# Kernel tuning notes

Hardware: AMD Instinct MI355X
Metric: run time of the kernel (lower is better)

## Reference

```python
import jax, jax.numpy as jnp
import numpy as np

B, IN_CH, N, DIM, PH, HID, K = 4, 128, 2048, 256, 64, 1024, 16
EPS = 1e-5


def conv1(x, w, b):
    # 1x1 Conv1d: x (B,C,N), w (O,C) -> (B,O,N)
    return jnp.einsum('oc,bcn->bon', w, x) + b[None, :, None]


def conv2(x, w, b):
    # 1x1 Conv2d: x (B,C,N,K), w (O,C) -> (B,O,N,K)
    return jnp.einsum('oc,bcnk->bonk', w, x) + b[None, :, None, None]


def bn2(x, g, beta, mean, var):
    # eval-mode BatchNorm2d over channel dim of (B,C,N,K)
    scale = g * jax.lax.rsqrt(var + EPS)
    return x * scale[None, :, None, None] + (beta - mean * scale)[None, :, None, None]


def query_knn(pos, k):
    # pos: (B,3,N). Returns (B,N,K) indices of k nearest neighbors (incl. self).
    p = jnp.transpose(pos, (0, 2, 1))                     # (B,N,3)
    sq = jnp.sum(p * p, axis=-1)                          # (B,N)
    dist = sq[:, :, None] + sq[:, None, :] - 2.0 * jnp.einsum('bnc,bmc->bnm', p, p)
    _, idx = jax.lax.top_k(-dist, k)                      # smallest distances first
    return idx


def group(feat, idx):
    # feat: (B,C,N), idx: (B,N,K) -> (B,C,N,K) where out[b,c,i,k]=feat[b,c,idx[b,i,k]]
    b, c, n = feat.shape
    k = idx.shape[-1]
    ib = jnp.broadcast_to(idx.reshape(b, 1, n * k), (b, c, n * k))
    return jnp.take_along_axis(feat, ib, axis=2).reshape(b, c, n, k)


def setup_inputs() -> dict:
    key = jax.random.key(0)
    ks = jax.random.split(key, 12)
    s = 0.02
    return {
        'x': jax.random.normal(ks[0], (B, IN_CH, N), jnp.float32),
        'pos': jax.random.normal(ks[1], (B, 3, N), jnp.float32),
        'ls_w': jax.random.normal(ks[2], (DIM, IN_CH), jnp.float32) * s,
        'ls_b': jnp.zeros((DIM,), jnp.float32),
        'kw': jax.random.normal(ks[3], (DIM, DIM), jnp.float32) * s,
        'kb': jnp.zeros((DIM,), jnp.float32),
        'qw': jax.random.normal(ks[4], (DIM, DIM), jnp.float32) * s,
        'qb': jnp.zeros((DIM,), jnp.float32),
        'vw': jax.random.normal(ks[5], (DIM, DIM), jnp.float32) * s,
        'vb': jnp.zeros((DIM,), jnp.float32),
        'pw1': jax.random.normal(ks[6], (PH, 3), jnp.float32) * s,
        'pb1': jnp.zeros((PH,), jnp.float32),
        'pg': jnp.ones((PH,), jnp.float32),
        'pbeta': jnp.zeros((PH,), jnp.float32),
        'pmean': jnp.zeros((PH,), jnp.float32),
        'pvar': jnp.ones((PH,), jnp.float32),
        'pw2': jax.random.normal(ks[7], (DIM, PH), jnp.float32) * s,
        'pb2': jnp.zeros((DIM,), jnp.float32),
        'aw1': jax.random.normal(ks[8], (HID, DIM), jnp.float32) * s,
        'ab1': jnp.zeros((HID,), jnp.float32),
        'ag': jnp.ones((HID,), jnp.float32),
        'abeta': jnp.zeros((HID,), jnp.float32),
        'amean': jnp.zeros((HID,), jnp.float32),
        'avar': jnp.ones((HID,), jnp.float32),
        'aw2': jax.random.normal(ks[9], (DIM, HID), jnp.float32) * s,
        'ab2': jnp.zeros((DIM,), jnp.float32),
        'lw': jax.random.normal(ks[10], (IN_CH, DIM), jnp.float32) * s,
        'lb': jnp.zeros((IN_CH,), jnp.float32),
    }


def reference(x, pos, ls_w, ls_b, kw, kb, qw, qb, vw, vb,
              pw1, pb1, pg, pbeta, pmean, pvar, pw2, pb2,
              aw1, ab1, ag, abeta, amean, avar, aw2, ab2, lw, lb):
    identity = x
    h = conv1(x, ls_w, ls_b)                              # (B,DIM,N)
    idx = query_knn(pos, K)                               # (B,N,K) int32
    key_f = group(conv1(h, kw, kb), idx)                  # (B,DIM,N,K)
    value = conv1(h, vw, vb)                              # (B,DIM,N)
    query = conv1(h, qw, qb)                              # (B,DIM,N)
    qk_rel = query[:, :, :, None] - key_f                 # (B,DIM,N,K)
    pos_rel = pos[:, :, :, None] - group(pos, idx)        # (B,3,N,K)
    pe = conv2(jax.nn.relu(bn2(conv2(pos_rel, pw1, pb1), pg, pbeta, pmean, pvar)), pw2, pb2)
    attn = conv2(jax.nn.relu(bn2(conv2(qk_rel + pe, aw1, ab1), ag, abeta, amean, avar)), aw2, ab2)
    attn = jax.nn.softmax(attn, axis=-1)                  # softmax over K
    val_g = group(value, idx) + pe                        # (B,DIM,N,K)
    agg = jnp.sum(attn * val_g, axis=-1)                  # (B,DIM,N)
    y = conv1(agg, lw, lb)                                # (B,IN_CH,N)
    return y + identity
```

## Files before the change

kernel.cpp:

```cpp
#include <hip/hip_runtime.h>
#include <hip/hip_bf16.h>
#include <math.h>

#define B_    4
#define CIN   128
#define NPTS  2048
#define DIM   256
#define PH    64
#define HIDN  1024
#define KNN_  16
#define BN    (B_*NPTS)
#define CC    (BN*KNN_)
#define QKV   768
#define EPS_  1e-5f

typedef __bf16 bf16;
typedef __bf16 bf16x8 __attribute__((ext_vector_type(8)));
typedef __bf16 bf16x4 __attribute__((ext_vector_type(4)));
typedef float  f32x4  __attribute__((ext_vector_type(4)));

__global__ __launch_bounds__(256) void prep_kernel(
    const float* __restrict__ ls_w, const float* __restrict__ qw,
    const float* __restrict__ kw,   const float* __restrict__ vw,
    const float* __restrict__ pw2,  const float* __restrict__ aw1,
    const float* __restrict__ aw2,  const float* __restrict__ lw,
    const float* __restrict__ qb,   const float* __restrict__ kb,
    const float* __restrict__ vb,
    const float* __restrict__ pb1,  const float* __restrict__ pg,
    const float* __restrict__ pbeta,const float* __restrict__ pmean,
    const float* __restrict__ pvar,
    const float* __restrict__ ab1,  const float* __restrict__ ag,
    const float* __restrict__ abeta,const float* __restrict__ amean,
    const float* __restrict__ avar,
    bf16* ls_wb, bf16* wqkvb, bf16* pw2b, bf16* aw1b, bf16* aw2b, bf16* lwb,
    float* pe_scale, float* pe_shift, float* at_scale, float* at_shift,
    float* bqkv)
{
  long e = (long)blockIdx.x * 256 + threadIdx.x;
  if (e < 32768)  { ls_wb[e] = (bf16)ls_w[e]; return; } e -= 32768;
  if (e < 196608) {
    int row = (int)(e >> 8), col = (int)(e & 255);
    float v = (row < 256) ? qw[row * 256 + col]
            : (row < 512) ? kw[(row - 256) * 256 + col]
                          : vw[(row - 512) * 256 + col];
    wqkvb[e] = (bf16)v; return;
  } e -= 196608;
  if (e < 16384)  { pw2b[e] = (bf16)pw2[e];  return; } e -= 16384;
  if (e < 262144) { aw1b[e] = (bf16)aw1[e];  return; } e -= 262144;
  if (e < 262144) { aw2b[e] = (bf16)aw2[e];  return; } e -= 262144;
  if (e < 32768)  { lwb[e]  = (bf16)lw[e];   return; } e -= 32768;
  if (e < 64) {
    float sc = pg[e] * rsqrtf(pvar[e] + EPS_);
    pe_scale[e] = sc;
    pe_shift[e] = sc * pb1[e] + pbeta[e] - pmean[e] * sc;
    return;
  } e -= 64;
  if (e < 1024) {
    float sc = ag[e] * rsqrtf(avar[e] + EPS_);
    at_scale[e] = sc;
    at_shift[e] = sc * ab1[e] + abeta[e] - amean[e] * sc;
    return;
  } e -= 1024;
  if (e < 768) {
    bqkv[e] = (e < 256) ? qb[e] : (e < 512) ? kb[e - 256] : vb[e - 512];
  }
}

__global__ __launch_bounds__(256) void transpose_x_kernel(
    const float* __restrict__ x, bf16* __restrict__ xT)
{
  long e = (long)blockIdx.x * 256 + threadIdx.x;
  int ch = (int)(e & (CIN - 1));
  long i = e >> 7;
  int n = (int)(i & (NPTS - 1));
  int b = (int)(i >> 11);
  xT[e] = (bf16)x[((long)b * CIN + ch) * NPTS + n];
}

__global__ __launch_bounds__(256) void knn_kernel(
    const float* __restrict__ pos, int* __restrict__ idx_out)
{
  __shared__ float px[NPTS], py[NPTS], pz[NPTS];
  const int tid = threadIdx.x;
  const int lane = tid & 63, wave = tid >> 6;
  const int q = blockIdx.x * 4 + wave;
  const int b = q >> 11;
  const int n = q & (NPTS - 1);
  const float* p = pos + (long)b * 3 * NPTS;
  for (int j = tid; j < NPTS; j += 256) {
    px[j] = p[j]; py[j] = p[NPTS + j]; pz[j] = p[2 * NPTS + j];
  }
  __syncthreads();
  float qx = px[n], qy = py[n], qz = pz[n];
  float qs = qx * qx + qy * qy + qz * qz;
  float d[32];
#pragma unroll
  for (int j = 0; j < 32; ++j) {
    int pt = j * 64 + lane;
    float x = px[pt], y = py[pt], z = pz[pt];
    float s2 = x * x + y * y + z * z;
    float dt = qx * x + qy * y + qz * z;
    d[j] = qs + s2 - 2.f * dt;
  }
  for (int r = 0; r < KNN_; ++r) {
    float bv = 1e30f; int bj = 0;
#pragma unroll
    for (int j = 0; j < 32; ++j)
      if (d[j] < bv) { bv = d[j]; bj = j; }
    int bi = bj * 64 + lane;
#pragma unroll
    for (int off = 32; off >= 1; off >>= 1) {
      float ov = __shfl_xor(bv, off);
      int   oi = __shfl_xor(bi, off);
      if (ov < bv || (ov == bv && oi < bi)) { bv = ov; bi = oi; }
    }
    if (lane == 0) idx_out[(long)q * KNN_ + r] = bi;
#pragma unroll
    for (int j = 0; j < 32; ++j)
      if (bi == j * 64 + lane) d[j] = 1e30f;
  }
}

template<int KD, bool OBF16>
__global__ __launch_bounds__(256) void gemmT_kernel(
    const bf16* __restrict__ inT, const bf16* __restrict__ Wb,
    const float* __restrict__ bias, void* __restrict__ outp, int O)
{
  const int tid = threadIdx.x;
  const int lane = tid & 63, wave = tid >> 6;
  const int row16 = lane & 15, grp = lane >> 4;
  const long i0 = (long)blockIdx.x * 64 + (wave & 1) * 32;
  const long o0 = (long)blockIdx.y * 64 + (wave >> 1) * 32;
  f32x4 acc[2][2] = {};
  const bf16* a0p = inT + (i0 + row16) * KD + grp * 8;
  const bf16* a1p = a0p + 16 * KD;
  const bf16* b0p = Wb + (o0 + row16) * KD + grp * 8;
  const bf16* b1p = b0p + 16 * KD;
#pragma unroll
  for (int ks = 0; ks < KD / 32; ++ks) {
    bf16x8 a0 = *(const bf16x8*)(a0p + ks * 32);
    bf16x8 a1 = *(const bf16x8*)(a1p + ks * 32);
    bf16x8 b0 = *(const bf16x8*)(b0p + ks * 32);
    bf16x8 b1 = *(const bf16x8*)(b1p + ks * 32);
    acc[0][0] = __builtin_amdgcn_mfma_f32_16x16x32_bf16(a0, b0, acc[0][0], 0, 0, 0);
    acc[0][1] = __builtin_amdgcn_mfma_f32_16x16x32_bf16(a0, b1, acc[0][1], 0, 0, 0);
    acc[1][0] = __builtin_amdgcn_mfma_f32_16x16x32_bf16(a1, b0, acc[1][0], 0, 0, 0);
    acc[1][1] = __builtin_amdgcn_mfma_f32_16x16x32_bf16(a1, b1, acc[1][1], 0, 0, 0);
  }
#pragma unroll
  for (int ot = 0; ot < 2; ++ot) {
    long o = o0 + ot * 16 + row16;
    float bv = bias[o];
#pragma unroll
    for (int it = 0; it < 2; ++it) {
#pragma unroll
      for (int r = 0; r < 4; ++r) {
        long i = i0 + it * 16 + grp * 4 + r;
        float v = acc[it][ot][r] + bv;
        if (OBF16) ((bf16*)outp)[i * O + o] = (bf16)v;
        else       ((float*)outp)[i * O + o] = v;
      }
    }
  }
}

__global__ __launch_bounds__(256) void gemmT_qkv_kernel(
    const bf16* __restrict__ inT, const bf16* __restrict__ Wb,
    const float* __restrict__ bias,
    bf16* __restrict__ qTb, bf16* __restrict__ kTb, bf16* __restrict__ vTb)
{
  const int tid = threadIdx.x;
  const int lane = tid & 63, wave = tid >> 6;
  const int row16 = lane & 15, grp = lane >> 4;
  const long i0 = (long)blockIdx.x * 64 + (wave & 1) * 32;
  const long o0 = (long)blockIdx.y * 64 + (wave >> 1) * 32;
  f32x4 acc[2][2] = {};
  const bf16* a0p = inT + (i0 + row16) * DIM + grp * 8;
  const bf16* a1p = a0p + 16 * DIM;
  const bf16* b0p = Wb + (o0 + row16) * DIM + grp * 8;
  const bf16* b1p = b0p + 16 * DIM;
#pragma unroll
  for (int ks = 0; ks < 8; ++ks) {
    bf16x8 a0 = *(const bf16x8*)(a0p + ks * 32);
    bf16x8 a1 = *(const bf16x8*)(a1p + ks * 32);
    bf16x8 b0 = *(const bf16x8*)(b0p + ks * 32);
    bf16x8 b1 = *(const bf16x8*)(b1p + ks * 32);
    acc[0][0] = __builtin_amdgcn_mfma_f32_16x16x32_bf16(a0, b0, acc[0][0], 0, 0, 0);
    acc[0][1] = __builtin_amdgcn_mfma_f32_16x16x32_bf16(a0, b1, acc[0][1], 0, 0, 0);
    acc[1][0] = __builtin_amdgcn_mfma_f32_16x16x32_bf16(a1, b0, acc[1][0], 0, 0, 0);
    acc[1][1] = __builtin_amdgcn_mfma_f32_16x16x32_bf16(a1, b1, acc[1][1], 0, 0, 0);
  }
#pragma unroll
  for (int ot = 0; ot < 2; ++ot) {
    long o = o0 + ot * 16 + row16;
    int third = (int)(o >> 8);
    bf16* outp = third == 0 ? qTb : third == 1 ? kTb : vTb;
    int oo = (int)(o & 255);
    float bv = bias[o];
#pragma unroll
    for (int it = 0; it < 2; ++it) {
#pragma unroll
      for (int r = 0; r < 4; ++r) {
        long i = i0 + it * 16 + grp * 4 + r;
        outp[i * DIM + oo] = (bf16)(acc[it][ot][r] + bv);
      }
    }
  }
}

__global__ __launch_bounds__(256, 3) void attn_fused_kernel(
    const bf16* __restrict__ qTb, const bf16* __restrict__ kTb,
    const bf16* __restrict__ vTb, const float* __restrict__ pos,
    const int* __restrict__ idx, const float* __restrict__ pw1,
    const float* __restrict__ pe_scale, const float* __restrict__ pe_shift,
    const bf16* __restrict__ pw2b, const float* __restrict__ pb2,
    const bf16* __restrict__ aw1b, const bf16* __restrict__ aw2b,
    const float* __restrict__ at_scale, const float* __restrict__ at_shift,
    const float* __restrict__ ab2, bf16* __restrict__ aggT)
{
  __shared__ __align__(16) bf16 u_lds[64][272];
  __shared__ __align__(16) bf16 tbuf[64 * 136];
  __shared__ float rel_lds[64][4];
  __shared__ int   idx_lds[64];
  bf16 (*t_lds)[136]  = (bf16(*)[136])tbuf;
  bf16 (*hid_lds)[72] = (bf16(*)[72])tbuf;

  const int tid = threadIdx.x;
  const int lane = tid & 63, wave = tid >> 6;
  const int row16 = lane & 15, grp = lane >> 4;
  const long c0 = (long)blockIdx.x * 64;
  const int bn0 = blockIdx.x * 4;
  const int b = bn0 >> 11;
  const float* pB = pos + (long)b * 3 * NPTS;
  const int os = wave * 64;
  const int hs = wave * 32;

  if (tid < 64) {
    int nb = idx[c0 + tid];
    idx_lds[tid] = nb;
    int n = (bn0 + (tid >> 4)) & (NPTS - 1);
    rel_lds[tid][0] = pB[n] - pB[nb];
    rel_lds[tid][1] = pB[NPTS + n] - pB[NPTS + nb];
    rel_lds[tid][2] = pB[2 * NPTS + n] - pB[2 * NPTS + nb];
  }
  __syncthreads();

  {
    int c = tid & 63, jq = tid >> 6;
    float rx = rel_lds[c][0], ry = rel_lds[c][1], rz = rel_lds[c][2];
#pragma unroll
    for (int jj = 0; jj < 16; ++jj) {
      int j = jq * 16 + jj;
      float v = pw1[j * 3] * rx + pw1[j * 3 + 1] * ry + pw1[j * 3 + 2] * rz;
      v = pe_scale[j] * v + pe_shift[j];
      hid_lds[c][j] = (bf16)fmaxf(v, 0.f);
    }
  }
  __syncthreads();

  {
    bf16x8 bw[2][4];
#pragma unroll
    for (int ks = 0; ks < 2; ++ks)
#pragma unroll
      for (int ot = 0; ot < 4; ++ot)
        bw[ks][ot] = *(const bf16x8*)(pw2b + (long)(os + ot * 16 + row16) * PH + ks * 32 + grp * 8);
#pragma unroll
    for (int ct = 0; ct < 4; ++ct) {
      f32x4 aT[4] = {};
#pragma unroll
      for (int ks = 0; ks < 2; ++ks) {
        bf16x8 ah = *(const bf16x8*)&hid_lds[ct * 16 + row16][ks * 32 + grp * 8];
#pragma unroll
        for (int ot = 0; ot < 4; ++ot)
          aT[ot] = __builtin_amdgcn_mfma_f32_16x16x32_bf16(bw[ks][ot], ah, aT[ot], 0, 0, 0);
      }
      int nb = idx_lds[ct * 16 + row16];
      const bf16* krow = kTb + ((long)b * NPTS + nb) * DIM + os;
      const bf16* qrow = qTb + (long)(bn0 + ct) * DIM + os;
#pragma unroll
      for (int ot = 0; ot < 4; ++ot) {
        int o4 = ot * 16 + grp * 4;
        bf16x4 k4 = *(const bf16x4*)(krow + o4);
        bf16x4 q4 = *(const bf16x4*)(qrow + o4);
        f32x4 pb4 = *(const f32x4*)&pb2[os + o4];
        bf16x4 u4;
#pragma unroll
        for (int r = 0; r < 4; ++r)
          u4[r] = (bf16)((float)q4[r] - (float)k4[r] + aT[ot][r] + pb4[r]);
        *(bf16x4*)&u_lds[ct * 16 + row16][os + o4] = u4;
      }
    }
  }
  __syncthreads();

  f32x4 acc2[4][4] = {};
  for (int jc = 0; jc < 8; ++jc) {
    const int hg = jc * 128 + hs;
#pragma unroll
    for (int jt = 0; jt < 2; ++jt) {
      f32x4 acc1[4] = {};
#pragma unroll
      for (int ks = 0; ks < 8; ++ks) {
        bf16x8 aw = *(const bf16x8*)(aw1b + (long)(hg + jt * 16 + row16) * DIM + ks * 32 + grp * 8);
#pragma unroll
        for (int ct = 0; ct < 4; ++ct) {
          bf16x8 bu = *(const bf16x8*)&u_lds[ct * 16 + row16][ks * 32 + grp * 8];
          acc1[ct] = __builtin_amdgcn_mfma_f32_16x16x32_bf16(aw, bu, acc1[ct], 0, 0, 0);
        }
      }
      int jb = hg + jt * 16 + grp * 4;
      f32x4 sc4 = *(const f32x4*)&at_scale[jb];
      f32x4 sh4 = *(const f32x4*)&at_shift[jb];
#pragma unroll
      for (int ct = 0; ct < 4; ++ct) {
        bf16x4 pk;
#pragma unroll
        for (int r = 0; r < 4; ++r) {
          float v = sc4[r] * acc1[ct][r] + sh4[r];
          pk[r] = (bf16)fmaxf(v, 0.f);
        }
        *(bf16x4*)&t_lds[ct * 16 + row16][hs + jt * 16 + grp * 4] = pk;
      }
    }
    __syncthreads();
#pragma unroll
    for (int ks2 = 0; ks2 < 4; ++ks2) {
      bf16x8 a2[4], b2;
#pragma unroll
      for (int ct = 0; ct < 4; ++ct)
        a2[ct] = *(const bf16x8*)&t_lds[ct * 16 + row16][ks2 * 32 + grp * 8];
#pragma unroll
      for (int ot = 0; ot < 4; ++ot) {
        b2 = *(const bf16x8*)(aw2b + (long)(os + ot * 16 + row16) * HIDN + jc * 128 + ks2 * 32 + grp * 8);
#pragma unroll
        for (int ct = 0; ct < 4; ++ct)
          acc2[ct][ot] = __builtin_amdgcn_mfma_f32_16x16x32_bf16(a2[ct], b2, acc2[ct][ot], 0, 0, 0);
      }
    }
    __syncthreads();
  }

  {
    int c = tid & 63, jq = tid >> 6;
    float rx = rel_lds[c][0], ry = rel_lds[c][1], rz = rel_lds[c][2];
#pragma unroll
    for (int jj = 0; jj < 16; ++jj) {
      int j = jq * 16 + jj;
      float v = pw1[j * 3] * rx + pw1[j * 3 + 1] * ry + pw1[j * 3 + 2] * rz;
      v = pe_scale[j] * v + pe_shift[j];
      hid_lds[c][j] = (bf16)fmaxf(v, 0.f);
    }
  }
  __syncthreads();

#pragma unroll
  for (int ct = 0; ct < 4; ++ct) {
    f32x4 accpe[4] = {};
#pragma unroll
    for (int ks = 0; ks < 2; ++ks) {
      bf16x8 ah = *(const bf16x8*)&hid_lds[ct * 16 + row16][ks * 32 + grp * 8];
#pragma unroll
      for (int ot = 0; ot < 4; ++ot) {
        bf16x8 bwv = *(const bf16x8*)(pw2b + (long)(os + ot * 16 + row16) * PH + ks * 32 + grp * 8);
        accpe[ot] = __builtin_amdgcn_mfma_f32_16x16x32_bf16(ah, bwv, accpe[ot], 0, 0, 0);
      }
    }
#pragma unroll
    for (int ot = 0; ot < 4; ++ot) {
      int o = os + ot * 16 + row16;
      float ab = ab2[o];
      float pb2v = pb2[o];
      float l[4];
      float m = -1e30f;
#pragma unroll
      for (int r = 0; r < 4; ++r) {
        l[r] = acc2[ct][ot][r] + ab;
        m = fmaxf(m, l[r]);
      }
      m = fmaxf(m, __shfl_xor(m, 16));
      m = fmaxf(m, __shfl_xor(m, 32));
      float s = 0.f;
#pragma unroll
      for (int r = 0; r < 4; ++r) { l[r] = expf(l[r] - m); s += l[r]; }
      s += __shfl_xor(s, 16);
      s += __shfl_xor(s, 32);
      float inv = 1.f / s;
      float agg = 0.f;
#pragma unroll
      for (int r = 0; r < 4; ++r) {
        int c = ct * 16 + grp * 4 + r;
        int nb = idx_lds[c];
        float vv = (float)vTb[((long)b * NPTS + nb) * DIM + o];
        agg += l[r] * (vv + accpe[ot][r] + pb2v);
      }
      agg *= inv;
      agg += __shfl_xor(agg, 16);
      agg += __shfl_xor(agg, 32);
      if (grp == 0) aggT[(long)(bn0 + ct) * DIM + o] = (bf16)agg;
    }
  }
}

__global__ __launch_bounds__(256) void final_kernel(
    const bf16* __restrict__ aggT, const bf16* __restrict__ lwb,
    const float* __restrict__ lb, const float* __restrict__ x,
    float* __restrict__ out)
{
  const int tid = threadIdx.x;
  const int lane = tid & 63, wave = tid >> 6;
  const int row16 = lane & 15, grp = lane >> 4;
  const long i0 = (long)blockIdx.x * 64 + (wave & 1) * 32;
  const int o0 = blockIdx.y * 64 + (wave >> 1) * 32;
  f32x4 acc[2][2] = {};
  const bf16* a0p = aggT + (i0 + row16) * DIM + grp * 8;
  const bf16* a1p = a0p + 16 * DIM;
  const bf16* b0p = lwb + (long)(o0 + row16) * DIM + grp * 8;
  const bf16* b1p = b0p + 16 * DIM;
#pragma unroll
  for (int ks = 0; ks < 8; ++ks) {
    bf16x8 a0 = *(const bf16x8*)(a0p + ks * 32);
    bf16x8 a1 = *(const bf16x8*)(a1p + ks * 32);
    bf16x8 b0 = *(const bf16x8*)(b0p + ks * 32);
    bf16x8 b1 = *(const bf16x8*)(b1p + ks * 32);
    acc[0][0] = __builtin_amdgcn_mfma_f32_16x16x32_bf16(a0, b0, acc[0][0], 0, 0, 0);
    acc[0][1] = __builtin_amdgcn_mfma_f32_16x16x32_bf16(a0, b1, acc[0][1], 0, 0, 0);
    acc[1][0] = __builtin_amdgcn_mfma_f32_16x16x32_bf16(a1, b0, acc[1][0], 0, 0, 0);
    acc[1][1] = __builtin_amdgcn_mfma_f32_16x16x32_bf16(a1, b1, acc[1][1], 0, 0, 0);
  }
#pragma unroll
  for (int ot = 0; ot < 2; ++ot) {
    int o = o0 + ot * 16 + row16;
    float bv = lb[o];
#pragma unroll
    for (int it = 0; it < 2; ++it) {
#pragma unroll
      for (int r = 0; r < 4; ++r) {
        long i = i0 + it * 16 + grp * 4 + r;
        int bb = (int)(i >> 11);
        int n = (int)(i & (NPTS - 1));
        long off = ((long)bb * CIN + o) * NPTS + n;
        out[off] = acc[it][ot][r] + bv + x[off];
      }
    }
  }
}

extern "C" void kernel_launch(void* const* d_in, const int* in_sizes, int n_in,
                              void* d_out, int out_size, void* d_ws, size_t ws_size,
                              hipStream_t stream)
{
  const float* x     = (const float*)d_in[0];
  const float* pos   = (const float*)d_in[1];
  const float* ls_w  = (const float*)d_in[2];
  const float* ls_b  = (const float*)d_in[3];
  const float* kw    = (const float*)d_in[4];
  const float* kb    = (const float*)d_in[5];
  const float* qw    = (const float*)d_in[6];
  const float* qb    = (const float*)d_in[7];
  const float* vw    = (const float*)d_in[8];
  const float* vb    = (const float*)d_in[9];
  const float* pw1   = (const float*)d_in[10];
  const float* pb1   = (const float*)d_in[11];
  const float* pg    = (const float*)d_in[12];
  const float* pbeta = (const float*)d_in[13];
  const float* pmean = (const float*)d_in[14];
  const float* pvar  = (const float*)d_in[15];
  const float* pw2   = (const float*)d_in[16];
  const float* pb2   = (const float*)d_in[17];
  const float* aw1   = (const float*)d_in[18];
  const float* ab1   = (const float*)d_in[19];
  const float* ag    = (const float*)d_in[20];
  const float* abeta = (const float*)d_in[21];
  const float* amean = (const float*)d_in[22];
  const float* avar  = (const float*)d_in[23];
  const float* aw2   = (const float*)d_in[24];
  const float* ab2   = (const float*)d_in[25];
  const float* lw    = (const float*)d_in[26];
  const float* lb    = (const float*)d_in[27];

  char* ws = (char*)d_ws;
  size_t off = 0;
  auto alloc = [&](size_t bytes) -> void* {
    void* p = ws + off;
    off = (off + bytes + 255) & ~(size_t)255;
    return p;
  };

  bf16* ls_wb = (bf16*)alloc(32768 * 2);
  bf16* wqkvb = (bf16*)alloc(196608 * 2);
  bf16* pw2b  = (bf16*)alloc(16384 * 2);
  bf16* aw1b  = (bf16*)alloc(262144 * 2);
  bf16* aw2b  = (bf16*)alloc(262144 * 2);
  bf16* lwb   = (bf16*)alloc(32768 * 2);
  float* pe_scale = (float*)alloc(64 * 4);
  float* pe_shift = (float*)alloc(64 * 4);
  float* at_scale = (float*)alloc(1024 * 4);
  float* at_shift = (float*)alloc(1024 * 4);
  float* bqkv = (float*)alloc(768 * 4);
  int*  idx  = (int*)alloc((size_t)CC * 4);
  bf16* xT   = (bf16*)alloc((size_t)BN * CIN * 2);
  bf16* hT   = (bf16*)alloc((size_t)BN * DIM * 2);
  bf16* qTb  = (bf16*)alloc((size_t)BN * DIM * 2);
  bf16* kTb  = (bf16*)alloc((size_t)BN * DIM * 2);
  bf16* vTb  = (bf16*)alloc((size_t)BN * DIM * 2);
  bf16* aggT = (bf16*)alloc((size_t)BN * DIM * 2);

  prep_kernel<<<dim3((804672 + 255) / 256), 256, 0, stream>>>(
      ls_w, qw, kw, vw, pw2, aw1, aw2, lw, qb, kb, vb,
      pb1, pg, pbeta, pmean, pvar, ab1, ag, abeta, amean, avar,
      ls_wb, wqkvb, pw2b, aw1b, aw2b, lwb,
      pe_scale, pe_shift, at_scale, at_shift, bqkv);

  transpose_x_kernel<<<dim3(BN * CIN / 256), 256, 0, stream>>>(x, xT);

  knn_kernel<<<dim3(BN / 4), 256, 0, stream>>>(pos, idx);

  gemmT_kernel<128, true><<<dim3(BN / 64, DIM / 64), 256, 0, stream>>>(xT, ls_wb, ls_b, hT, DIM);

  gemmT_qkv_kernel<<<dim3(BN / 64, QKV / 64), 256, 0, stream>>>(hT, wqkvb, bqkv, qTb, kTb, vTb);

  attn_fused_kernel<<<dim3(CC / 64), 256, 0, stream>>>(
      qTb, kTb, vTb, pos, idx, pw1, pe_scale, pe_shift, pw2b, pb2,
      aw1b, aw2b, at_scale, at_shift, ab2, aggT);

  final_kernel<<<dim3(BN / 64, CIN / 64), 256, 0, stream>>>(aggT, lwb, lb, x, (float*)d_out);
}
```

Baseline: 555.9 us.

## Switch attention MLP GEMMs to FP8 MFMA with fp8 weights and activations

Converts aw1/aw2 weights to fp8 e4m3 in prep and quantises the u and hidden activations to fp8 in LDS, using fp8 16x16x32 MFMA instead of bf16. Hidden chunks widen from 128 to 256 columns, halving barrier count. This cuts memory and LDS bytes and uses the higher-rate fp8 matrix path, but adds quantisation error that may exceed tolerance.

```diff
diff --git a/kernel.cpp b/kernel.cpp
--- a/kernel.cpp
+++ b/kernel.cpp
@@ -18,6 +18,14 @@
 typedef __bf16 bf16x8 __attribute__((ext_vector_type(8)));
 typedef __bf16 bf16x4 __attribute__((ext_vector_type(4)));
 typedef float  f32x4  __attribute__((ext_vector_type(4)));
+typedef unsigned char u8;
+typedef long long i64;
+
+static __device__ __forceinline__ int pack4_fp8(float a, float b, float c, float d) {
+  int v = __builtin_amdgcn_cvt_pk_fp8_f32(a, b, 0, false);
+  v = __builtin_amdgcn_cvt_pk_fp8_f32(c, d, v, true);
+  return v;
+}
 
 __global__ __launch_bounds__(256) void prep_kernel(
     const float* __restrict__ ls_w, const float* __restrict__ qw,
@@ -32,7 +40,7 @@
     const float* __restrict__ ab1,  const float* __restrict__ ag,
     const float* __restrict__ abeta,const float* __restrict__ amean,
     const float* __restrict__ avar,
-    bf16* ls_wb, bf16* wqkvb, bf16* pw2b, bf16* aw1b, bf16* aw2b, bf16* lwb,
+    bf16* ls_wb, bf16* wqkvb, bf16* pw2b, u8* aw1f8, u8* aw2f8, bf16* lwb,
     float* pe_scale, float* pe_shift, float* at_scale, float* at_shift,
     float* bqkv)
 {
@@ -46,8 +54,14 @@
     wqkvb[e] = (bf16)v; return;
   } e -= 196608;
   if (e < 16384)  { pw2b[e] = (bf16)pw2[e];  return; } e -= 16384;
-  if (e < 262144) { aw1b[e] = (bf16)aw1[e];  return; } e -= 262144;
-  if (e < 262144) { aw2b[e] = (bf16)aw2[e];  return; } e -= 262144;
+  if (e < 262144) {
+    int p = __builtin_amdgcn_cvt_pk_fp8_f32(aw1[e], 0.f, 0, false);
+    aw1f8[e] = (u8)p; return;
+  } e -= 262144;
+  if (e < 262144) {
+    int p = __builtin_amdgcn_cvt_pk_fp8_f32(aw2[e], 0.f, 0, false);
+    aw2f8[e] = (u8)p; return;
+  } e -= 262144;
   if (e < 32768)  { lwb[e]  = (bf16)lw[e];   return; } e -= 32768;
   if (e < 64) {
     float sc = pg[e] * rsqrtf(pvar[e] + EPS_);
@@ -214,15 +228,15 @@
     const int* __restrict__ idx, const float* __restrict__ pw1,
     const float* __restrict__ pe_scale, const float* __restrict__ pe_shift,
     const bf16* __restrict__ pw2b, const float* __restrict__ pb2,
-    const bf16* __restrict__ aw1b, const bf16* __restrict__ aw2b,
+    const u8* __restrict__ aw1f8, const u8* __restrict__ aw2f8,
     const float* __restrict__ at_scale, const float* __restrict__ at_shift,
     const float* __restrict__ ab2, bf16* __restrict__ aggT)
 {
-  __shared__ __align__(16) bf16 u_lds[64][272];
-  __shared__ __align__(16) bf16 tbuf[64 * 136];
+  __shared__ __align__(16) u8 u_lds[64][264];
+  __shared__ __align__(16) u8 tbuf[64 * 264];
   __shared__ float rel_lds[64][4];
   __shared__ int   idx_lds[64];
-  bf16 (*t_lds)[136]  = (bf16(*)[136])tbuf;
+  u8   (*t_lds)[264]  = (u8(*)[264])tbuf;
   bf16 (*hid_lds)[72] = (bf16(*)[72])tbuf;
 
   const int tid = threadIdx.x;
@@ -233,7 +247,7 @@
   const int b = bn0 >> 11;
   const float* pB = pos + (long)b * 3 * NPTS;
   const int os = wave * 64;
-  const int hs = wave * 32;
+  const int hs = wave * 64;
 
   if (tid < 64) {
     int nb = idx[c0 + tid];
@@ -284,58 +298,58 @@
         bf16x4 k4 = *(const bf16x4*)(krow + o4);
         bf16x4 q4 = *(const bf16x4*)(qrow + o4);
         f32x4 pb4 = *(const f32x4*)&pb2[os + o4];
-        bf16x4 u4;
-#pragma unroll
-        for (int r = 0; r < 4; ++r)
-          u4[r] = (bf16)((float)q4[r] - (float)k4[r] + aT[ot][r] + pb4[r]);
-        *(bf16x4*)&u_lds[ct * 16 + row16][os + o4] = u4;
+        int u32 = pack4_fp8(
+            (float)q4[0] - (float)k4[0] + aT[ot][0] + pb4[0],
+            (float)q4[1] - (float)k4[1] + aT[ot][1] + pb4[1],
+            (float)q4[2] - (float)k4[2] + aT[ot][2] + pb4[2],
+            (float)q4[3] - (float)k4[3] + aT[ot][3] + pb4[3]);
+        *(int*)&u_lds[ct * 16 + row16][os + o4] = u32;
       }
     }
   }
   __syncthreads();
 
   f32x4 acc2[4][4] = {};
-  for (int jc = 0; jc < 8; ++jc) {
-    const int hg = jc * 128 + hs;
-#pragma unroll
-    for (int jt = 0; jt < 2; ++jt) {
+  for (int jc = 0; jc < 4; ++jc) {
+#pragma unroll
+    for (int jt = 0; jt < 4; ++jt) {
+      const int jrow = jc * 256 + hs + jt * 16 + row16;
       f32x4 acc1[4] = {};
 #pragma unroll
       for (int ks = 0; ks < 8; ++ks) {
-        bf16x8 aw = *(const bf16x8*)(aw1b + (long)(hg + jt * 16 + row16) * DIM + ks * 32 + grp * 8);
+        i64 aw = *(const i64*)(aw1f8 + (long)jrow * DIM + ks * 32 + grp * 8);
 #pragma unroll
         for (int ct = 0; ct < 4; ++ct) {
-          bf16x8 bu = *(const bf16x8*)&u_lds[ct * 16 + row16][ks * 32 + grp * 8];
-          acc1[ct] = __builtin_amdgcn_mfma_f32_16x16x32_bf16(aw, bu, acc1[ct], 0, 0, 0);
+          i64 bu = *(const i64*)&u_lds[ct * 16 + row16][ks * 32 + grp * 8];
+          acc1[ct] = __builtin_amdgcn_mfma_f32_16x16x32_fp8_fp8(aw, bu, acc1[ct], 0, 0, 0);
         }
       }
-      int jb = hg + jt * 16 + grp * 4;
+      int jb = jc * 256 + hs + jt * 16 + grp * 4;
       f32x4 sc4 = *(const f32x4*)&at_scale[jb];
       f32x4 sh4 = *(const f32x4*)&at_shift[jb];
 #pragma unroll
       for (int ct = 0; ct < 4; ++ct) {
-        bf16x4 pk;
-#pragma unroll
-        for (int r = 0; r < 4; ++r) {
-          float v = sc4[r] * acc1[ct][r] + sh4[r];
-          pk[r] = (bf16)fmaxf(v, 0.f);
-        }
-        *(bf16x4*)&t_lds[ct * 16 + row16][hs + jt * 16 + grp * 4] = pk;
+        int pk = pack4_fp8(
+            fmaxf(sc4[0] * acc1[ct][0] + sh4[0], 0.f),
+            fmaxf(sc4[1] * acc1[ct][1] + sh4[1], 0.f),
+            fmaxf(sc4[2] * acc1[ct][2] + sh4[2], 0.f),
+            fmaxf(sc4[3] * acc1[ct][3] + sh4[3], 0.f));
+        *(int*)&t_lds[ct * 16 + row16][hs + jt * 16 + grp * 4] = pk;
       }
     }
     __syncthreads();
 #pragma unroll
-    for (int ks2 = 0; ks2 < 4; ++ks2) {
-      bf16x8 a2[4], b2;
+    for (int ks2 = 0; ks2 < 8; ++ks2) {
+      i64 a2[4];
 #pragma unroll
       for (int ct = 0; ct < 4; ++ct)
-        a2[ct] = *(const bf16x8*)&t_lds[ct * 16 + row16][ks2 * 32 + grp * 8];
+        a2[ct] = *(const i64*)&t_lds[ct * 16 + row16][ks2 * 32 + grp * 8];
 #pragma unroll
       for (int ot = 0; ot < 4; ++ot) {
-        b2 = *(const bf16x8*)(aw2b + (long)(os + ot * 16 + row16) * HIDN + jc * 128 + ks2 * 32 + grp * 8);
+        i64 b2 = *(const i64*)(aw2f8 + (long)(os + ot * 16 + row16) * HIDN + jc * 256 + ks2 * 32 + grp * 8);
 #pragma unroll
         for (int ct = 0; ct < 4; ++ct)
-          acc2[ct][ot] = __builtin_amdgcn_mfma_f32_16x16x32_bf16(a2[ct], b2, acc2[ct][ot], 0, 0, 0);
+          acc2[ct][ot] = __builtin_amdgcn_mfma_f32_16x16x32_fp8_fp8(a2[ct], b2, acc2[ct][ot], 0, 0, 0);
       }
     }
     __syncthreads();
@@ -490,8 +504,8 @@
   bf16* ls_wb = (bf16*)alloc(32768 * 2);
   bf16* wqkvb = (bf16*)alloc(196608 * 2);
   bf16* pw2b  = (bf16*)alloc(16384 * 2);
-  bf16* aw1b  = (bf16*)alloc(262144 * 2);
-  bf16* aw2b  = (bf16*)alloc(262144 * 2);
+  u8*   aw1f8 = (u8*)alloc(262144);
+  u8*   aw2f8 = (u8*)alloc(262144);
   bf16* lwb   = (bf16*)alloc(32768 * 2);
   float* pe_scale = (float*)alloc(64 * 4);
   float* pe_shift = (float*)alloc(64 * 4);
@@ -509,7 +523,7 @@
   prep_kernel<<<dim3((804672 + 255) / 256), 256, 0, stream>>>(
       ls_w, qw, kw, vw, pw2, aw1, aw2, lw, qb, kb, vb,
       pb1, pg, pbeta, pmean, pvar, ab1, ag, abeta, amean, avar,
-      ls_wb, wqkvb, pw2b, aw1b, aw2b, lwb,
+      ls_wb, wqkvb, pw2b, aw1f8, aw2f8, lwb,
       pe_scale, pe_shift, at_scale, at_shift, bqkv);
 
   transpose_x_kernel<<<dim3(BN * CIN / 256), 256, 0, stream>>>(x, xT);
@@ -522,7 +536,7 @@
 
   attn_fused_kernel<<<dim3(CC / 64), 256, 0, stream>>>(
       qTb, kTb, vTb, pos, idx, pw1, pe_scale, pe_shift, pw2b, pb2,
-      aw1b, aw2b, at_scale, at_shift, ab2, aggT);
+      aw1f8, aw2f8, at_scale, at_shift, ab2, aggT);
 
   final_kernel<<<dim3(BN / 64, CIN / 64), 256, 0, stream>>>(aggT, lwb, lb, x, (float*)d_out);
 }
```

After: 580.9 us. 1.04x slower.
